# Kernel tuning notes

Measured on AMD Instinct MI355X. Metric: run time of the kernel, lower is better.

## Reference

```python
import jax, jax.numpy as jnp
import numpy as np

B, L, D_MODEL, VQ_DIM, K_CODES = 4, 2048, 1024, 64, 8192
EMA_K, EMA_GAMMA = 5, 0.995


def _huber(a, b):
    # HuberLoss(reduction='none'), delta=1.0
    d = a - b
    ad = jnp.abs(d)
    return jnp.where(ad < 1.0, 0.5 * d * d, ad - 0.5)


def setup_inputs() -> dict:
    key = jax.random.key(0)
    ks = jax.random.split(key, 6)
    h = jax.random.normal(ks[0], (B, L, D_MODEL), dtype=jnp.float32)
    attn_mask = jnp.ones((B, L), dtype=jnp.float32)
    proj_w = jax.random.normal(ks[1], (D_MODEL, VQ_DIM), dtype=jnp.float32) / np.sqrt(D_MODEL)
    proj_b = jnp.zeros((VQ_DIM,), dtype=jnp.float32)
    proj_inv_w = jax.random.normal(ks[2], (VQ_DIM, D_MODEL), dtype=jnp.float32) / np.sqrt(VQ_DIM)
    proj_inv_b = jnp.zeros((D_MODEL,), dtype=jnp.float32)
    emb_weight = jax.random.uniform(ks[3], (K_CODES, VQ_DIM), dtype=jnp.float32,
                                    minval=-1.0 / K_CODES, maxval=1.0 / K_CODES)
    count = jnp.zeros((K_CODES,), dtype=jnp.float32)
    return {"h": h, "attn_mask": attn_mask, "proj_w": proj_w, "proj_b": proj_b,
            "proj_inv_w": proj_inv_w, "proj_inv_b": proj_inv_b,
            "emb_weight": emb_weight, "count": count}


def reference(h, attn_mask, proj_w, proj_b, proj_inv_w, proj_inv_b, emb_weight, count):
    # project + L2-normalize tokens
    hp = h @ proj_w + proj_b                                   # [B, L, vq]
    hp = hp / jnp.linalg.norm(hp, axis=-1, keepdims=True)
    h_flat = hp.reshape(-1, VQ_DIM)                            # [N, vq]
    # L2-normalize codebook (in-place .data normalization in torch)
    E = emb_weight / jnp.linalg.norm(emb_weight, axis=-1, keepdims=True)  # [K, vq]
    # squared-distance via norm expansion
    distances = (jnp.sum(h_flat ** 2, axis=1, keepdims=True)
                 + jnp.sum(E ** 2, axis=1)
                 - 2.0 * h_flat @ E.T)                         # [N, K]
    m = attn_mask.reshape(-1, 1)
    distances = distances * m + 1e7 * (1.0 - m)
    code = jnp.argmin(distances, axis=1).reshape(B, L)         # [B, L]
    quantized = E[code]                                        # gather [B, L, vq]
    # straight-through estimator
    q_ste = hp + jax.lax.stop_gradient(quantized - hp)
    # usage count buffer update (unique+bincount == scatter-add of ones)
    new_count = count.at[code.reshape(-1)].add(1.0)
    # EMA codebook update (train mode): top-k nearest tokens per code
    neg_top, topk_ids = jax.lax.top_k((-distances).T, EMA_K)   # [K, k]
    h_feat = h_flat[topk_ids].mean(axis=1)                     # [K, vq]
    update_mask = jnp.abs(neg_top).min(axis=1) > 0.1           # [K]
    updated = E * EMA_GAMMA + h_feat * (1.0 - EMA_GAMMA)
    new_emb = jnp.where(update_mask[:, None], updated, E)
    # commitment / codebook loss (Huber both ways), masked mean
    loss = _huber(jax.lax.stop_gradient(hp), q_ste) + 0.25 * _huber(hp, jax.lax.stop_gradient(q_ste))
    mw = attn_mask[:, :, None]
    vq_loss = ((loss * mw).sum(axis=1) / mw.sum(axis=1)).mean()
    q_out = q_ste @ proj_inv_w + proj_inv_b                    # [B, L, d_model]
    return q_out, code, vq_loss, new_emb, new_count
```

## Files before the change

kernel.cpp:

```cpp
#include <hip/hip_runtime.h>
#include <float.h>


typedef __attribute__((ext_vector_type(8)))  short bf16x8;
typedef __attribute__((ext_vector_type(16))) float f32x16;

__device__ __forceinline__ unsigned short f2bf(float x) {
  unsigned u = __float_as_uint(x);
  unsigned r = (u + 0x7fffu + ((u >> 16) & 1u)) >> 16;
  return (unsigned short)r;
}
__device__ __forceinline__ float bf2f(unsigned short b) {
  return __uint_as_float(((unsigned)b) << 16);
}
__device__ __forceinline__ size_t frag_off(int e, int ks, int lh) {
  return ((size_t)((((e >> 5) * 4 + ks) * 2 + lh) * 32 + (e & 31))) * 8;
}

__device__ __forceinline__ void kins5(unsigned& s0, unsigned& s1, unsigned& s2,
                                      unsigned& s3, unsigned& s4, unsigned k) {
  unsigned t = k, m;
  m = min(s0, t); t = max(s0, t); s0 = m;
  m = min(s1, t); t = max(s1, t); s1 = m;
  m = min(s2, t); t = max(s2, t); s2 = m;
  m = min(s3, t); t = max(s3, t); s3 = m;
  s4 = min(s4, t);
}
__device__ __forceinline__ void lins5(float& d0, float& d1, float& d2,
                                      float& d3, float& d4, int& i0, int& i1,
                                      int& i2, int& i3, int& i4, float dv,
                                      int iv) {
  if (dv < d4 || (dv == d4 && iv < i4)) {
    d4 = dv; i4 = iv;
    if (d4 < d3 || (d4 == d3 && i4 < i3)) { float t = d3; d3 = d4; d4 = t; int u = i3; i3 = i4; i4 = u; }
    if (d3 < d2 || (d3 == d2 && i3 < i2)) { float t = d2; d2 = d3; d3 = t; int u = i2; i2 = i3; i3 = u; }
    if (d2 < d1 || (d2 == d1 && i2 < i1)) { float t = d1; d1 = d2; d2 = t; int u = i1; i1 = i2; i2 = u; }
    if (d1 < d0 || (d1 == d0 && i1 < i0)) { float t = d0; d0 = d1; d1 = t; int u = i0; i0 = i1; i1 = u; }
  }
}

__global__ __launch_bounds__(256) void k_proj(
    const float* __restrict__ h, const float* __restrict__ w,
    const float* __restrict__ bias, float* __restrict__ hp_norm,
    float* __restrict__ h2, unsigned short* __restrict__ hpH,
    unsigned short* __restrict__ hpL) {
  __shared__ __align__(16) float hs[16 * 68];
  __shared__ __align__(16) float ws[64 * 64];
  const int tid = threadIdx.x;
  const int tb = blockIdx.x * 16;
  const int tok = tid >> 4;
  const int dimg = tid & 15;
  const float4* h4 = (const float4*)h;
  const float4* w4 = (const float4*)w;
  float4* ws4 = (float4*)ws;
  float4 acc = {0.f, 0.f, 0.f, 0.f};
  for (int ch = 0; ch < 16; ++ch) {
    __syncthreads();
    *(float4*)&hs[tok * 68 + dimg * 4] = h4[(size_t)(tb + tok) * 256 + ch * 16 + dimg];
#pragma unroll
    for (int i = 0; i < 4; ++i) {
      int idx = tid + i * 256;
      int k = idx >> 4, dq = idx & 15;
      ws4[k * 16 + dq] = w4[(size_t)(ch * 64 + k) * 16 + dq];
    }
    __syncthreads();
#pragma unroll 8
    for (int k = 0; k < 64; ++k) {
      float hv = hs[tok * 68 + k];
      float4 wv = *(const float4*)&ws[k * 64 + dimg * 4];
      acc.x = fmaf(hv, wv.x, acc.x);
      acc.y = fmaf(hv, wv.y, acc.y);
      acc.z = fmaf(hv, wv.z, acc.z);
      acc.w = fmaf(hv, wv.w, acc.w);
    }
  }
  const float4 bv = ((const float4*)bias)[dimg];
  acc.x += bv.x; acc.y += bv.y; acc.z += bv.z; acc.w += bv.w;
  float sq = acc.x * acc.x + acc.y * acc.y + acc.z * acc.z + acc.w * acc.w;
#pragma unroll
  for (int o = 1; o <= 8; o <<= 1) sq += __shfl_xor(sq, o, 64);
  float nrm = sqrtf(sq);
  float4 vn;
  vn.x = acc.x / nrm; vn.y = acc.y / nrm; vn.z = acc.z / nrm; vn.w = acc.w / nrm;
  ((float4*)hp_norm)[(size_t)(tb + tok) * 16 + dimg] = vn;
  unsigned short hx = f2bf(vn.x), hy = f2bf(vn.y), hz = f2bf(vn.z), hw = f2bf(vn.w);
  uint2 hi_pack, lo_pack;
  hi_pack.x = (unsigned)hx | ((unsigned)hy << 16);
  hi_pack.y = (unsigned)hz | ((unsigned)hw << 16);
  lo_pack.x = (unsigned)f2bf(vn.x - bf2f(hx)) | ((unsigned)f2bf(vn.y - bf2f(hy)) << 16);
  lo_pack.y = (unsigned)f2bf(vn.z - bf2f(hz)) | ((unsigned)f2bf(vn.w - bf2f(hw)) << 16);
  {
    int ks = dimg >> 2, lh = (dimg >> 1) & 1, half = dimg & 1;
    size_t off = frag_off(tb + tok, ks, lh) + half * 4;
    *(uint2*)(hpH + off) = hi_pack;
    *(uint2*)(hpL + off) = lo_pack;
  }
  float s2 = vn.x * vn.x + vn.y * vn.y + vn.z * vn.z + vn.w * vn.w;
#pragma unroll
  for (int o = 1; o <= 8; o <<= 1) s2 += __shfl_xor(s2, o, 64);
  if (dimg == 0) h2[tb + tok] = s2;
}

__global__ __launch_bounds__(256) void k_enorm(
    const float* __restrict__ emb, float* __restrict__ E,
    float* __restrict__ e2, unsigned short* __restrict__ EH,
    unsigned short* __restrict__ EL,
    const float* __restrict__ cnt, float* __restrict__ ncnt,
    const float* __restrict__ wiv, unsigned short* __restrict__ wTH,
    unsigned short* __restrict__ wTL) {
  __shared__ float tile[64][65];
  const int b = blockIdx.x;
  const int tid = threadIdx.x;
  if (b >= 2080) {
    const int n0 = (b - 2080) * 64;
    const float4* w4 = (const float4*)wiv;
#pragma unroll
    for (int i = 0; i < 4; ++i) {
      int idx = tid + i * 256;
      int k = idx >> 4, nq = idx & 15;
      float4 v = w4[k * 256 + (n0 >> 2) + nq];
      tile[nq * 4 + 0][k] = v.x;
      tile[nq * 4 + 1][k] = v.y;
      tile[nq * 4 + 2][k] = v.z;
      tile[nq * 4 + 3][k] = v.w;
    }
    __syncthreads();
    const int n = tid >> 2;
    const int k0 = (tid & 3) * 16;
#pragma unroll
    for (int j = 0; j < 16; j += 4) {
      int k = k0 + j;
      float x0 = tile[n][k], x1 = tile[n][k + 1], x2 = tile[n][k + 2],
            x3 = tile[n][k + 3];
      unsigned short h0 = f2bf(x0), h1 = f2bf(x1), h2_ = f2bf(x2), h3 = f2bf(x3);
      uint2 hp_, lp_;
      hp_.x = (unsigned)h0 | ((unsigned)h1 << 16);
      hp_.y = (unsigned)h2_ | ((unsigned)h3 << 16);
      lp_.x = (unsigned)f2bf(x0 - bf2f(h0)) | ((unsigned)f2bf(x1 - bf2f(h1)) << 16);
      lp_.y = (unsigned)f2bf(x2 - bf2f(h2_)) | ((unsigned)f2bf(x3 - bf2f(h3)) << 16);
      size_t off = frag_off(n0 + n, k >> 4, (k >> 3) & 1) + (k & 7);
      *(uint2*)(wTH + off) = hp_;
      *(uint2*)(wTL + off) = lp_;
    }
    return;
  }
  if (b >= 2048) {
    int i = (b - 2048) * 256 + tid;
    ncnt[i] = cnt[i];
    return;
  }
  const int c = b * 4 + (tid >> 6);
  const int lane = tid & 63;
  float v = emb[(size_t)c * 64 + lane];
  float sq = v * v;
#pragma unroll
  for (int o = 32; o > 0; o >>= 1) sq += __shfl_xor(sq, o, 64);
  float vn = v / sqrtf(sq);
  E[(size_t)c * 64 + lane] = vn;
  unsigned short hb = f2bf(vn);
  size_t off = frag_off(c, lane >> 4, (lane >> 3) & 1) + (lane & 7);
  EH[off] = hb;
  EL[off] = f2bf(vn - bf2f(hb));
  float s2 = vn * vn;
#pragma unroll
  for (int o = 32; o > 0; o >>= 1) s2 += __shfl_xor(s2, o, 64);
  if (lane == 0) e2[c] = s2;
}

__global__ __launch_bounds__(512, 4) void k_argmin(
    const unsigned short* __restrict__ hpH, const unsigned short* __restrict__ hpL,
    const unsigned short* __restrict__ EHg, const unsigned short* __restrict__ ELg,
    const float* __restrict__ e2g,
    float* __restrict__ amin_d, int* __restrict__ amin_c) {
  __shared__ __align__(16) unsigned char buf[2][16384];
  __shared__ float e2l[1024];
  __shared__ float mD[2][128];
  __shared__ int   mC[2][128];
  const int tid = threadIdx.x;
  const int w = tid >> 6, lane = tid & 63;
  const int l31 = lane & 31, lh = lane >> 5;
  const int rowg = w >> 1, colg = w & 1;
  const int tok_base = blockIdx.x * 128;
  const int cstrip = blockIdx.y * 1024;
  const int row_t = tok_base + rowg * 32 + l31;
  bf16x8 aH[4], aL[4];
#pragma unroll
  for (int ks = 0; ks < 4; ++ks) {
    aH[ks] = *(const bf16x8*)(hpH + frag_off(row_t, ks, lh));
    aL[ks] = *(const bf16x8*)(hpL + frag_off(row_t, ks, lh));
  }
  e2l[tid] = e2g[cstrip + tid];
  e2l[tid + 512] = e2g[cstrip + tid + 512];
  float bu[16]; int bc[16];
#pragma unroll
  for (int r = 0; r < 16; ++r) { bu[r] = FLT_MAX; bc[r] = 0x7fffffff; }
  bf16x8 rH, rL;
  {
    size_t gb = (size_t)(blockIdx.y * 32) * 2048 + (size_t)tid * 8;
    rH = *(const bf16x8*)(EHg + gb);
    rL = *(const bf16x8*)(ELg + gb);
    *(bf16x8*)(buf[0] + tid * 16) = rH;
    *(bf16x8*)(buf[0] + 8192 + tid * 16) = rL;
  }
  __syncthreads();
  for (int ch = 0; ch < 16; ++ch) {
    if (ch < 15) {
      size_t gb = (size_t)(blockIdx.y * 32 + (ch + 1) * 2) * 2048 + (size_t)tid * 8;
      rH = *(const bf16x8*)(EHg + gb);
      rL = *(const bf16x8*)(ELg + gb);
    }
    const unsigned char* bcur = buf[ch & 1];
    f32x16 acc = {};
#pragma unroll
    for (int ks = 0; ks < 4; ++ks) {
      const int boff = ((colg * 8 + ks * 2 + lh) * 32 + l31) * 16;
      bf16x8 bL = *(const bf16x8*)(bcur + 8192 + boff);
      bf16x8 bH = *(const bf16x8*)(bcur + boff);
      acc = __builtin_amdgcn_mfma_f32_32x32x16_bf16(aL[ks], bL, acc, 0, 0, 0);
      acc = __builtin_amdgcn_mfma_f32_32x32x16_bf16(aL[ks], bH, acc, 0, 0, 0);
      acc = __builtin_amdgcn_mfma_f32_32x32x16_bf16(aH[ks], bL, acc, 0, 0, 0);
      acc = __builtin_amdgcn_mfma_f32_32x32x16_bf16(aH[ks], bH, acc, 0, 0, 0);
    }
    const int mycode = cstrip + ch * 64 + colg * 32 + l31;
    const float e2c = e2l[ch * 64 + colg * 32 + l31];
#pragma unroll
    for (int r = 0; r < 16; ++r) {
      float u = fmaf(-2.f, acc[r], e2c);
      if (u < bu[r]) { bu[r] = u; bc[r] = mycode; }
    }
    if (ch < 15) {
      *(bf16x8*)(buf[(ch + 1) & 1] + tid * 16) = rH;
      *(bf16x8*)(buf[(ch + 1) & 1] + 8192 + tid * 16) = rL;
    }
    __syncthreads();
  }
#pragma unroll
  for (int r = 0; r < 16; ++r) {
#pragma unroll
    for (int o = 1; o <= 16; o <<= 1) {
      float ou = __shfl_xor(bu[r], o, 64);
      int oc = __shfl_xor(bc[r], o, 64);
      if (ou < bu[r] || (ou == bu[r] && oc < bc[r])) { bu[r] = ou; bc[r] = oc; }
    }
  }
  if (l31 == 0) {
#pragma unroll
    for (int r = 0; r < 16; ++r) {
      const int roff = rowg * 32 + (r & 3) + 8 * (r >> 2) + 4 * lh;
      mD[colg][roff] = bu[r];
      mC[colg][roff] = bc[r];
    }
  }
  __syncthreads();
  if (tid < 128) {
    float d0 = mD[0][tid], d1 = mD[1][tid];
    int c0 = mC[0][tid], c1 = mC[1][tid];
    if (d1 < d0 || (d1 == d0 && c1 < c0)) { d0 = d1; c0 = c1; }
    const int t = tok_base + tid;
    amin_d[(size_t)t * 8 + blockIdx.y] = d0;
    amin_c[(size_t)t * 8 + blockIdx.y] = c0;
  }
}

__global__ __launch_bounds__(512, 4) void k_top5(
    const unsigned short* __restrict__ hpH, const unsigned short* __restrict__ hpL,
    const unsigned short* __restrict__ EHg, const unsigned short* __restrict__ ELg,
    const float* __restrict__ h2g, const float* __restrict__ e2g,
    const float* __restrict__ maskg,
    float* __restrict__ t5d, int* __restrict__ t5i) {
  __shared__ __align__(16) unsigned char buf[2][16384];
  __shared__ __align__(16) float Pl[1024];
  __shared__ float sD[4][2][32][5];
  __shared__ int   sI[4][2][32][5];
  const int tid = threadIdx.x;
  const int w = tid >> 6, lane = tid & 63;
  const int l31 = lane & 31, lh = lane >> 5;
  const int rowg = w >> 2, colg = w & 3;
  const int code_t = blockIdx.x * 128 + colg * 32 + l31;
  const int tstrip = blockIdx.y * 1024;
  bf16x8 bH[4], bL[4];
#pragma unroll
  for (int ks = 0; ks < 4; ++ks) {
    bH[ks] = *(const bf16x8*)(EHg + frag_off(code_t, ks, lh));
    bL[ks] = *(const bf16x8*)(ELg + frag_off(code_t, ks, lh));
  }
  {
    int t0 = tid, t1 = tid + 512;
    float m0 = maskg[tstrip + t0], m1 = maskg[tstrip + t1];
    Pl[t0] = fmaf(h2g[tstrip + t0], m0, 1.0e7f * (1.f - m0) + 4.0f);
    Pl[t1] = fmaf(h2g[tstrip + t1], m1, 1.0e7f * (1.f - m1) + 4.0f);
  }
  unsigned s0 = 0xFFFFFFFFu, s1 = 0xFFFFFFFFu, s2 = 0xFFFFFFFFu,
           s3 = 0xFFFFFFFFu, s4 = 0xFFFFFFFFu;
  bf16x8 rH, rL;
  {
    size_t gb = (size_t)(blockIdx.y * 32) * 2048 + (size_t)tid * 8;
    rH = *(const bf16x8*)(hpH + gb);
    rL = *(const bf16x8*)(hpL + gb);
    *(bf16x8*)(buf[0] + tid * 16) = rH;
    *(bf16x8*)(buf[0] + 8192 + tid * 16) = rL;
  }
  __syncthreads();
  for (int ch = 0; ch < 16; ++ch) {
    if (ch < 15) {
      size_t gb = (size_t)(blockIdx.y * 32 + (ch + 1) * 2) * 2048 + (size_t)tid * 8;
      rH = *(const bf16x8*)(hpH + gb);
      rL = *(const bf16x8*)(hpL + gb);
    }
    const unsigned char* bcur = buf[ch & 1];
    f32x16 acc = {};
#pragma unroll
    for (int ks = 0; ks < 4; ++ks) {
      const int aoff = ((rowg * 8 + ks * 2 + lh) * 32 + l31) * 16;
      bf16x8 aL = *(const bf16x8*)(bcur + 8192 + aoff);
      bf16x8 aH = *(const bf16x8*)(bcur + aoff);
      acc = __builtin_amdgcn_mfma_f32_32x32x16_bf16(aL, bL[ks], acc, 0, 0, 0);
      acc = __builtin_amdgcn_mfma_f32_32x32x16_bf16(aL, bH[ks], acc, 0, 0, 0);
      acc = __builtin_amdgcn_mfma_f32_32x32x16_bf16(aH, bL[ks], acc, 0, 0, 0);
      acc = __builtin_amdgcn_mfma_f32_32x32x16_bf16(aH, bH[ks], acc, 0, 0, 0);
    }
    const int rowb = ch * 64 + rowg * 32 + 4 * lh;
    const unsigned encb = (unsigned)(ch << 4);
#pragma unroll
    for (int rq = 0; rq < 4; ++rq) {
      float4 pl = *(const float4*)&Pl[rowb + 8 * rq];
      float kx = fmaf(-2.f, acc[4 * rq + 0], pl.x);
      kins5(s0, s1, s2, s3, s4,
            (__float_as_uint(kx) & 0xFFFFFF00u) | (encb + 4 * rq + 0));
      float ky = fmaf(-2.f, acc[4 * rq + 1], pl.y);
      kins5(s0, s1, s2, s3, s4,
            (__float_as_uint(ky) & 0xFFFFFF00u) | (encb + 4 * rq + 1));
      float kz = fmaf(-2.f, acc[4 * rq + 2], pl.z);
      kins5(s0, s1, s2, s3, s4,
            (__float_as_uint(kz) & 0xFFFFFF00u) | (encb + 4 * rq + 2));
      float kw = fmaf(-2.f, acc[4 * rq + 3], pl.w);
      kins5(s0, s1, s2, s3, s4,
            (__float_as_uint(kw) & 0xFFFFFF00u) | (encb + 4 * rq + 3));
    }
    if (ch < 15) {
      *(bf16x8*)(buf[(ch + 1) & 1] + tid * 16) = rH;
      *(bf16x8*)(buf[(ch + 1) & 1] + 8192 + tid * 16) = rL;
    }
    __syncthreads();
  }
  float td0, td1, td2, td3, td4;
  int ti0, ti1, ti2, ti3, ti4;
  {
    auto dec = [&](unsigned k, float& d, int& i) {
      d = __uint_as_float(k & 0xFFFFFF00u);
      int enc = (int)(k & 255u);
      int r = enc & 15, chh = enc >> 4;
      i = tstrip + chh * 64 + rowg * 32 + lh * 4 + (r & 3) + 8 * (r >> 2);
    };
    dec(s0, td0, ti0); dec(s1, td1, ti1); dec(s2, td2, ti2);
    dec(s3, td3, ti3); dec(s4, td4, ti4);
  }
  {
    float od0 = __shfl_xor(td0, 32, 64), od1 = __shfl_xor(td1, 32, 64),
          od2 = __shfl_xor(td2, 32, 64), od3 = __shfl_xor(td3, 32, 64),
          od4 = __shfl_xor(td4, 32, 64);
    int oi0 = __shfl_xor(ti0, 32, 64), oi1 = __shfl_xor(ti1, 32, 64),
        oi2 = __shfl_xor(ti2, 32, 64), oi3 = __shfl_xor(ti3, 32, 64),
        oi4 = __shfl_xor(ti4, 32, 64);
    lins5(td0, td1, td2, td3, td4, ti0, ti1, ti2, ti3, ti4, od0, oi0);
    lins5(td0, td1, td2, td3, td4, ti0, ti1, ti2, ti3, ti4, od1, oi1);
    lins5(td0, td1, td2, td3, td4, ti0, ti1, ti2, ti3, ti4, od2, oi2);
    lins5(td0, td1, td2, td3, td4, ti0, ti1, ti2, ti3, ti4, od3, oi3);
    lins5(td0, td1, td2, td3, td4, ti0, ti1, ti2, ti3, ti4, od4, oi4);
  }
  if (lane < 32) {
    sD[colg][rowg][l31][0] = td0; sD[colg][rowg][l31][1] = td1;
    sD[colg][rowg][l31][2] = td2; sD[colg][rowg][l31][3] = td3;
    sD[colg][rowg][l31][4] = td4;
    sI[colg][rowg][l31][0] = ti0; sI[colg][rowg][l31][1] = ti1;
    sI[colg][rowg][l31][2] = ti2; sI[colg][rowg][l31][3] = ti3;
    sI[colg][rowg][l31][4] = ti4;
  }
  __syncthreads();
  if (tid < 128) {
    const int cg = tid >> 5, cl = tid & 31;
    float rd0 = sD[cg][0][cl][0], rd1 = sD[cg][0][cl][1],
          rd2 = sD[cg][0][cl][2], rd3 = sD[cg][0][cl][3],
          rd4 = sD[cg][0][cl][4];
    int ri0 = sI[cg][0][cl][0], ri1 = sI[cg][0][cl][1],
        ri2 = sI[cg][0][cl][2], ri3 = sI[cg][0][cl][3],
        ri4 = sI[cg][0][cl][4];
#pragma unroll
    for (int s = 0; s < 5; ++s)
      lins5(rd0, rd1, rd2, rd3, rd4, ri0, ri1, ri2, ri3, ri4,
            sD[cg][1][cl][s], sI[cg][1][cl][s]);
    const int code = blockIdx.x * 128 + tid;
    const float sh = e2g[code] - 4.0f;
    size_t gb = (size_t)code * 40 + (size_t)blockIdx.y * 5;
    t5d[gb + 0] = rd0 + sh; t5i[gb + 0] = ri0;
    t5d[gb + 1] = rd1 + sh; t5i[gb + 1] = ri1;
    t5d[gb + 2] = rd2 + sh; t5i[gb + 2] = ri2;
    t5d[gb + 3] = rd3 + sh; t5i[gb + 3] = ri3;
    t5d[gb + 4] = rd4 + sh; t5i[gb + 4] = ri4;
  }
}

__global__ __launch_bounds__(256) void k_code(
    const float* __restrict__ amin_d, const int* __restrict__ amin_c,
    const float* __restrict__ hp, const float* __restrict__ E,
    const float* __restrict__ maskg,
    float* __restrict__ code_f, int* __restrict__ code_i,
    float* __restrict__ newcount, float* __restrict__ loss_tok) {
  const int wid = threadIdx.x >> 6;
  const int lane = threadIdx.x & 63;
  const int t = blockIdx.x * 4 + wid;
  float d = FLT_MAX;
  int c = 0x7fffffff;
  if (lane < 8) {
    d = amin_d[(size_t)t * 8 + lane];
    c = amin_c[(size_t)t * 8 + lane];
  }
#pragma unroll
  for (int o = 1; o <= 4; o <<= 1) {
    float od = __shfl_xor(d, o, 64);
    int oc = __shfl_xor(c, o, 64);
    if (od < d || (od == d && oc < c)) { d = od; c = oc; }
  }
  c = __shfl(c, 0, 64);
  if (maskg[t] == 0.f) c = 0;
  float a = hp[(size_t)t * 64 + lane];
  float e = E[(size_t)c * 64 + lane];
  float q = a + (e - a);
  float df = a - q;
  float ad = fabsf(df);
  float l = ad < 1.f ? 0.5f * df * df : ad - 0.5f;
#pragma unroll
  for (int o = 32; o > 0; o >>= 1) l += __shfl_xor(l, o, 64);
  if (lane == 0) {
    code_f[t] = (float)c;
    code_i[t] = c;
    loss_tok[t] = l;
    atomicAdd(&newcount[c], 1.0f);
  }
}

__global__ __launch_bounds__(256, 2) void k_qout(
    const int* __restrict__ code_i,
    const unsigned short* __restrict__ EH, const unsigned short* __restrict__ EL,
    const unsigned short* __restrict__ wTH, const unsigned short* __restrict__ wTL,
    const float* __restrict__ bias, float* __restrict__ qout) {
  const int tid = threadIdx.x;
  const int w = tid >> 6, lane = tid & 63;
  const int l31 = lane & 31, lh = lane >> 5;
  const int rowg = w >> 1, colg = w & 1;
  const int tok_base = blockIdx.x * 64;
  const int col_base = blockIdx.y * 64;
  const int row_t = tok_base + rowg * 32 + l31;
  const int c = code_i[row_t];
  const int n = col_base + colg * 32 + l31;
  bf16x8 aH[4], aL[4], bH[4], bL[4];
#pragma unroll
  for (int ks = 0; ks < 4; ++ks) {
    aH[ks] = *(const bf16x8*)(EH + frag_off(c, ks, lh));
    aL[ks] = *(const bf16x8*)(EL + frag_off(c, ks, lh));
    bH[ks] = *(const bf16x8*)(wTH + frag_off(n, ks, lh));
    bL[ks] = *(const bf16x8*)(wTL + frag_off(n, ks, lh));
  }
  f32x16 c0 = {}, c1 = {}, c2 = {}, c3 = {};
#pragma unroll
  for (int ks = 0; ks < 4; ++ks) {
    c0 = __builtin_amdgcn_mfma_f32_32x32x16_bf16(aL[ks], bL[ks], c0, 0, 0, 0);
    c1 = __builtin_amdgcn_mfma_f32_32x32x16_bf16(aL[ks], bH[ks], c1, 0, 0, 0);
    c2 = __builtin_amdgcn_mfma_f32_32x32x16_bf16(aH[ks], bL[ks], c2, 0, 0, 0);
    c3 = __builtin_amdgcn_mfma_f32_32x32x16_bf16(aH[ks], bH[ks], c3, 0, 0, 0);
  }
  const float bc = bias[n];
#pragma unroll
  for (int r = 0; r < 16; ++r) {
    int row = rowg * 32 + (r & 3) + 8 * (r >> 2) + 4 * lh;
    float dot = ((c0[r] + c1[r]) + c2[r]) + c3[r];
    qout[(size_t)(tok_base + row) * 1024 + n] = dot + bc;
  }
}

__global__ __launch_bounds__(256) void k_emb(
    const float* __restrict__ t5d, const int* __restrict__ t5i,
    const float* __restrict__ hp, const float* __restrict__ E,
    float* __restrict__ newemb,
    const float* __restrict__ loss_tok, const float* __restrict__ maskg,
    float* __restrict__ vq) {
  __shared__ float S[256], M[256];
  const int tid = threadIdx.x;
  if (blockIdx.x == 2048) {
    float s = 0.f, m = 0.f;
    const int base = tid * 32;
    for (int i = 0; i < 32; ++i) {
      float mm = maskg[base + i];
      s = fmaf(loss_tok[base + i], mm, s);
      m += mm;
    }
    S[tid] = s; M[tid] = m;
    __syncthreads();
    if (tid == 0) {
      float tot = 0.f;
      for (int b = 0; b < 4; ++b) {
        float sb = 0.f, mb = 0.f;
        for (int i = 0; i < 64; ++i) { sb += S[b * 64 + i]; mb += M[b * 64 + i]; }
        tot += sb / mb;
      }
      vq[0] = tot * 1.25f / 256.0f;
    }
    return;
  }
  const int wid = tid >> 6;
  const int lane = tid & 63;
  const int c = blockIdx.x * 4 + wid;
  float d = FLT_MAX;
  int idx = 0x7fffffff;
  if (lane < 40) {
    d = t5d[(size_t)c * 40 + lane];
    idx = t5i[(size_t)c * 40 + lane];
  }
  float seld[5]; int sel[5];
#pragma unroll
  for (int r = 0; r < 5; ++r) {
    float bd = d; int bi = idx;
#pragma unroll
    for (int o = 1; o <= 32; o <<= 1) {
      float od = __shfl_xor(bd, o, 64);
      int oi = __shfl_xor(bi, o, 64);
      if (od < bd || (od == bd && oi < bi)) { bd = od; bi = oi; }
    }
    seld[r] = bd; sel[r] = bi;
    if (idx == bi) d = FLT_MAX;
  }
  float m5 = fabsf(seld[0]);
#pragma unroll
  for (int r = 1; r < 5; ++r) m5 = fminf(m5, fabsf(seld[r]));
  float hf = 0.f;
#pragma unroll
  for (int r = 0; r < 5; ++r) hf += hp[(size_t)sel[r] * 64 + lane];
  hf = hf / 5.0f;
  float ev = E[(size_t)c * 64 + lane];
  float outv = (m5 > 0.1f) ? (ev * 0.995f + hf * (float)(1.0 - 0.995)) : ev;
  newemb[(size_t)c * 64 + lane] = outv;
}

extern "C" void kernel_launch(void* const* d_in, const int* in_sizes, int n_in,
                              void* d_out, int out_size, void* d_ws,
                              size_t ws_size, hipStream_t stream) {
  (void)in_sizes; (void)n_in; (void)out_size; (void)ws_size;
  const float* h          = (const float*)d_in[0];
  const float* mask       = (const float*)d_in[1];
  const float* proj_w     = (const float*)d_in[2];
  const float* proj_b     = (const float*)d_in[3];
  const float* proj_inv_w = (const float*)d_in[4];
  const float* proj_inv_b = (const float*)d_in[5];
  const float* emb        = (const float*)d_in[6];
  const float* count      = (const float*)d_in[7];

  float* out      = (float*)d_out;
  float* q_out    = out;
  float* code_f   = out + 8388608;
  float* vq       = out + 8396800;
  float* newemb   = out + 8396801;
  float* newcount = out + 8921089;

  float* ws = (float*)d_ws;
  float* hp_norm        = ws;
  float* h2             = ws + 524288;
  float* E              = ws + 532480;
  float* e2             = ws + 1056768;
  unsigned short* hpH   = (unsigned short*)(ws + 1064960);
  unsigned short* hpL   = (unsigned short*)(ws + 1327104);
  unsigned short* EH    = (unsigned short*)(ws + 1589248);
  unsigned short* EL    = (unsigned short*)(ws + 1851392);
  unsigned short* wTH   = (unsigned short*)(ws + 2113536);
  unsigned short* wTL   = (unsigned short*)(ws + 2146304);
  float* amin_d         = ws + 2179072;
  int*   amin_c         = (int*)(ws + 2244608);
  int*   code_i         = (int*)(ws + 2310144);
  float* t5d            = ws + 2318336;
  int*   t5i            = (int*)(ws + 2646016);
  float* loss_tok       = ws + 2973696;

  k_proj<<<512, 256, 0, stream>>>(h, proj_w, proj_b, hp_norm, h2, hpH, hpL);
  k_enorm<<<2096, 256, 0, stream>>>(emb, E, e2, EH, EL, count, newcount,
                                    proj_inv_w, wTH, wTL);
  k_argmin<<<dim3(64, 8), 512, 0, stream>>>(hpH, hpL, EH, EL, e2,
                                            amin_d, amin_c);
  k_top5<<<dim3(64, 8), 512, 0, stream>>>(hpH, hpL, EH, EL, h2, e2, mask,
                                          t5d, t5i);
  k_code<<<2048, 256, 0, stream>>>(amin_d, amin_c, hp_norm, E, mask,
                                   code_f, code_i, newcount, loss_tok);
  k_qout<<<dim3(128, 16), 256, 0, stream>>>(code_i, EH, EL, wTH, wTL,
                                            proj_inv_b, q_out);
  k_emb<<<2049, 256, 0, stream>>>(t5d, t5i, hp_norm, E, newemb,
                                  loss_tok, mask, vq);
}
```

Baseline: 155.4 us.

## Split distance kernels into 16 strips and stage tiles via direct global-to-LDS loads

The argmin and top-5 kernels now split the reduction dimension into 16 strips instead of 8, doubling the grid to 1024 blocks with half the chunks per block. Tile staging uses global_load_lds so data goes straight into shared memory without passing through registers, and the reduction scratch arrays now reuse the staging buffer to cut shared-memory use. The downstream merge kernels are changed to combine 16 partial results per token and 80 candidates per code. The aim is more parallelism, more resident blocks per CU and lower register pressure. The cost is more partial results to write and merge, and reliance on the async LDS load finishing before the barrier.

```diff
diff --git a/kernel.cpp b/kernel.cpp
--- a/kernel.cpp
+++ b/kernel.cpp
@@ -4,6 +4,11 @@
 
 typedef __attribute__((ext_vector_type(8)))  short bf16x8;
 typedef __attribute__((ext_vector_type(16))) float f32x16;
+
+#define GLDS16(gp, lp)                                              \
+  __builtin_amdgcn_global_load_lds(                                 \
+      (const __attribute__((address_space(1))) void*)(gp),          \
+      (__attribute__((address_space(3))) void*)(lp), 16, 0, 0)
 
 __device__ __forceinline__ unsigned short f2bf(float x) {
   unsigned u = __float_as_uint(x);
@@ -172,16 +177,18 @@
     const unsigned short* __restrict__ EHg, const unsigned short* __restrict__ ELg,
     const float* __restrict__ e2g,
     float* __restrict__ amin_d, int* __restrict__ amin_c) {
-  __shared__ __align__(16) unsigned char buf[2][16384];
-  __shared__ float e2l[1024];
-  __shared__ float mD[2][128];
-  __shared__ int   mC[2][128];
+  __shared__ __align__(16) unsigned char smem[2 * 16384 + 2048];
+  unsigned char* buf0 = smem;
+  unsigned char* buf1 = smem + 16384;
+  float* e2l = (float*)(smem + 32768);
+  float* mD = (float*)smem;
+  int*   mC = (int*)(smem + 1024);
   const int tid = threadIdx.x;
   const int w = tid >> 6, lane = tid & 63;
   const int l31 = lane & 31, lh = lane >> 5;
   const int rowg = w >> 1, colg = w & 1;
   const int tok_base = blockIdx.x * 128;
-  const int cstrip = blockIdx.y * 1024;
+  const int cstrip = blockIdx.y * 512;
   const int row_t = tok_base + rowg * 32 + l31;
   bf16x8 aH[4], aL[4];
 #pragma unroll
@@ -190,26 +197,23 @@
     aL[ks] = *(const bf16x8*)(hpL + frag_off(row_t, ks, lh));
   }
   e2l[tid] = e2g[cstrip + tid];
-  e2l[tid + 512] = e2g[cstrip + tid + 512];
   float bu[16]; int bc[16];
 #pragma unroll
   for (int r = 0; r < 16; ++r) { bu[r] = FLT_MAX; bc[r] = 0x7fffffff; }
-  bf16x8 rH, rL;
   {
-    size_t gb = (size_t)(blockIdx.y * 32) * 2048 + (size_t)tid * 8;
-    rH = *(const bf16x8*)(EHg + gb);
-    rL = *(const bf16x8*)(ELg + gb);
-    *(bf16x8*)(buf[0] + tid * 16) = rH;
-    *(bf16x8*)(buf[0] + 8192 + tid * 16) = rL;
+    size_t gb = (size_t)(blockIdx.y * 16) * 2048 + (size_t)tid * 8;
+    GLDS16(EHg + gb, buf0 + tid * 16);
+    GLDS16(ELg + gb, buf0 + 8192 + tid * 16);
   }
   __syncthreads();
-  for (int ch = 0; ch < 16; ++ch) {
-    if (ch < 15) {
-      size_t gb = (size_t)(blockIdx.y * 32 + (ch + 1) * 2) * 2048 + (size_t)tid * 8;
-      rH = *(const bf16x8*)(EHg + gb);
-      rL = *(const bf16x8*)(ELg + gb);
-    }
-    const unsigned char* bcur = buf[ch & 1];
+  for (int ch = 0; ch < 8; ++ch) {
+    const unsigned char* bcur = (ch & 1) ? buf1 : buf0;
+    unsigned char* bnxt = (ch & 1) ? buf0 : buf1;
+    if (ch < 7) {
+      size_t gb = (size_t)(blockIdx.y * 16 + (ch + 1) * 2) * 2048 + (size_t)tid * 8;
+      GLDS16(EHg + gb, bnxt + tid * 16);
+      GLDS16(ELg + gb, bnxt + 8192 + tid * 16);
+    }
     f32x16 acc = {};
 #pragma unroll
     for (int ks = 0; ks < 4; ++ks) {
@@ -228,10 +232,6 @@
       float u = fmaf(-2.f, acc[r], e2c);
       if (u < bu[r]) { bu[r] = u; bc[r] = mycode; }
     }
-    if (ch < 15) {
-      *(bf16x8*)(buf[(ch + 1) & 1] + tid * 16) = rH;
-      *(bf16x8*)(buf[(ch + 1) & 1] + 8192 + tid * 16) = rL;
-    }
     __syncthreads();
   }
 #pragma unroll
@@ -247,18 +247,18 @@
 #pragma unroll
     for (int r = 0; r < 16; ++r) {
       const int roff = rowg * 32 + (r & 3) + 8 * (r >> 2) + 4 * lh;
-      mD[colg][roff] = bu[r];
-      mC[colg][roff] = bc[r];
+      mD[colg * 128 + roff] = bu[r];
+      mC[colg * 128 + roff] = bc[r];
     }
   }
   __syncthreads();
   if (tid < 128) {
-    float d0 = mD[0][tid], d1 = mD[1][tid];
-    int c0 = mC[0][tid], c1 = mC[1][tid];
+    float d0 = mD[tid], d1 = mD[128 + tid];
+    int c0 = mC[tid], c1 = mC[128 + tid];
     if (d1 < d0 || (d1 == d0 && c1 < c0)) { d0 = d1; c0 = c1; }
     const int t = tok_base + tid;
-    amin_d[(size_t)t * 8 + blockIdx.y] = d0;
-    amin_c[(size_t)t * 8 + blockIdx.y] = c0;
+    amin_d[(size_t)t * 16 + blockIdx.y] = d0;
+    amin_c[(size_t)t * 16 + blockIdx.y] = c0;
   }
 }
 
@@ -268,16 +268,18 @@
     const float* __restrict__ h2g, const float* __restrict__ e2g,
     const float* __restrict__ maskg,
     float* __restrict__ t5d, int* __restrict__ t5i) {
-  __shared__ __align__(16) unsigned char buf[2][16384];
-  __shared__ __align__(16) float Pl[1024];
-  __shared__ float sD[4][2][32][5];
-  __shared__ int   sI[4][2][32][5];
+  __shared__ __align__(16) unsigned char smem[2 * 16384 + 2048];
+  unsigned char* buf0 = smem;
+  unsigned char* buf1 = smem + 16384;
+  float* Pl = (float*)(smem + 32768);
+  float* sD = (float*)smem;
+  int*   sI = (int*)(smem + 5120);
   const int tid = threadIdx.x;
   const int w = tid >> 6, lane = tid & 63;
   const int l31 = lane & 31, lh = lane >> 5;
   const int rowg = w >> 2, colg = w & 3;
   const int code_t = blockIdx.x * 128 + colg * 32 + l31;
-  const int tstrip = blockIdx.y * 1024;
+  const int tstrip = blockIdx.y * 512;
   bf16x8 bH[4], bL[4];
 #pragma unroll
   for (int ks = 0; ks < 4; ++ks) {
@@ -285,29 +287,25 @@
     bL[ks] = *(const bf16x8*)(ELg + frag_off(code_t, ks, lh));
   }
   {
-    int t0 = tid, t1 = tid + 512;
-    float m0 = maskg[tstrip + t0], m1 = maskg[tstrip + t1];
-    Pl[t0] = fmaf(h2g[tstrip + t0], m0, 1.0e7f * (1.f - m0) + 4.0f);
-    Pl[t1] = fmaf(h2g[tstrip + t1], m1, 1.0e7f * (1.f - m1) + 4.0f);
+    float m0 = maskg[tstrip + tid];
+    Pl[tid] = fmaf(h2g[tstrip + tid], m0, 1.0e7f * (1.f - m0) + 4.0f);
   }
   unsigned s0 = 0xFFFFFFFFu, s1 = 0xFFFFFFFFu, s2 = 0xFFFFFFFFu,
            s3 = 0xFFFFFFFFu, s4 = 0xFFFFFFFFu;
-  bf16x8 rH, rL;
   {
-    size_t gb = (size_t)(blockIdx.y * 32) * 2048 + (size_t)tid * 8;
-    rH = *(const bf16x8*)(hpH + gb);
-    rL = *(const bf16x8*)(hpL + gb);
-    *(bf16x8*)(buf[0] + tid * 16) = rH;
-    *(bf16x8*)(buf[0] + 8192 + tid * 16) = rL;
+    size_t gb = (size_t)(blockIdx.y * 16) * 2048 + (size_t)tid * 8;
+    GLDS16(hpH + gb, buf0 + tid * 16);
+    GLDS16(hpL + gb, buf0 + 8192 + tid * 16);
   }
   __syncthreads();
-  for (int ch = 0; ch < 16; ++ch) {
-    if (ch < 15) {
-      size_t gb = (size_t)(blockIdx.y * 32 + (ch + 1) * 2) * 2048 + (size_t)tid * 8;
-      rH = *(const bf16x8*)(hpH + gb);
-      rL = *(const bf16x8*)(hpL + gb);
-    }
-    const unsigned char* bcur = buf[ch & 1];
+  for (int ch = 0; ch < 8; ++ch) {
+    const unsigned char* bcur = (ch & 1) ? buf1 : buf0;
+    unsigned char* bnxt = (ch & 1) ? buf0 : buf1;
+    if (ch < 7) {
+      size_t gb = (size_t)(blockIdx.y * 16 + (ch + 1) * 2) * 2048 + (size_t)tid * 8;
+      GLDS16(hpH + gb, bnxt + tid * 16);
+      GLDS16(hpL + gb, bnxt + 8192 + tid * 16);
+    }
     f32x16 acc = {};
 #pragma unroll
     for (int ks = 0; ks < 4; ++ks) {
@@ -337,10 +335,6 @@
       kins5(s0, s1, s2, s3, s4,
             (__float_as_uint(kw) & 0xFFFFFF00u) | (encb + 4 * rq + 3));
     }
-    if (ch < 15) {
-      *(bf16x8*)(buf[(ch + 1) & 1] + tid * 16) = rH;
-      *(bf16x8*)(buf[(ch + 1) & 1] + 8192 + tid * 16) = rL;
-    }
     __syncthreads();
   }
   float td0, td1, td2, td3, td4;
@@ -369,29 +363,26 @@
     lins5(td0, td1, td2, td3, td4, ti0, ti1, ti2, ti3, ti4, od4, oi4);
   }
   if (lane < 32) {
-    sD[colg][rowg][l31][0] = td0; sD[colg][rowg][l31][1] = td1;
-    sD[colg][rowg][l31][2] = td2; sD[colg][rowg][l31][3] = td3;
-    sD[colg][rowg][l31][4] = td4;
-    sI[colg][rowg][l31][0] = ti0; sI[colg][rowg][l31][1] = ti1;
-    sI[colg][rowg][l31][2] = ti2; sI[colg][rowg][l31][3] = ti3;
-    sI[colg][rowg][l31][4] = ti4;
+    float* sd = sD + (((colg * 2 + rowg) * 32) + l31) * 5;
+    int* si = sI + (((colg * 2 + rowg) * 32) + l31) * 5;
+    sd[0] = td0; sd[1] = td1; sd[2] = td2; sd[3] = td3; sd[4] = td4;
+    si[0] = ti0; si[1] = ti1; si[2] = ti2; si[3] = ti3; si[4] = ti4;
   }
   __syncthreads();
   if (tid < 128) {
     const int cg = tid >> 5, cl = tid & 31;
-    float rd0 = sD[cg][0][cl][0], rd1 = sD[cg][0][cl][1],
-          rd2 = sD[cg][0][cl][2], rd3 = sD[cg][0][cl][3],
-          rd4 = sD[cg][0][cl][4];
-    int ri0 = sI[cg][0][cl][0], ri1 = sI[cg][0][cl][1],
-        ri2 = sI[cg][0][cl][2], ri3 = sI[cg][0][cl][3],
-        ri4 = sI[cg][0][cl][4];
+    const float* s0p = sD + ((cg * 2 + 0) * 32 + cl) * 5;
+    const int* s0i = sI + ((cg * 2 + 0) * 32 + cl) * 5;
+    const float* s1p = sD + ((cg * 2 + 1) * 32 + cl) * 5;
+    const int* s1i = sI + ((cg * 2 + 1) * 32 + cl) * 5;
+    float rd0 = s0p[0], rd1 = s0p[1], rd2 = s0p[2], rd3 = s0p[3], rd4 = s0p[4];
+    int ri0 = s0i[0], ri1 = s0i[1], ri2 = s0i[2], ri3 = s0i[3], ri4 = s0i[4];
 #pragma unroll
     for (int s = 0; s < 5; ++s)
-      lins5(rd0, rd1, rd2, rd3, rd4, ri0, ri1, ri2, ri3, ri4,
-            sD[cg][1][cl][s], sI[cg][1][cl][s]);
+      lins5(rd0, rd1, rd2, rd3, rd4, ri0, ri1, ri2, ri3, ri4, s1p[s], s1i[s]);
     const int code = blockIdx.x * 128 + tid;
     const float sh = e2g[code] - 4.0f;
-    size_t gb = (size_t)code * 40 + (size_t)blockIdx.y * 5;
+    size_t gb = (size_t)code * 80 + (size_t)blockIdx.y * 5;
     t5d[gb + 0] = rd0 + sh; t5i[gb + 0] = ri0;
     t5d[gb + 1] = rd1 + sh; t5i[gb + 1] = ri1;
     t5d[gb + 2] = rd2 + sh; t5i[gb + 2] = ri2;
@@ -411,12 +402,12 @@
   const int t = blockIdx.x * 4 + wid;
   float d = FLT_MAX;
   int c = 0x7fffffff;
-  if (lane < 8) {
-    d = amin_d[(size_t)t * 8 + lane];
-    c = amin_c[(size_t)t * 8 + lane];
-  }
-#pragma unroll
-  for (int o = 1; o <= 4; o <<= 1) {
+  if (lane < 16) {
+    d = amin_d[(size_t)t * 16 + lane];
+    c = amin_c[(size_t)t * 16 + lane];
+  }
+#pragma unroll
+  for (int o = 1; o <= 8; o <<= 1) {
     float od = __shfl_xor(d, o, 64);
     int oc = __shfl_xor(c, o, 64);
     if (od < d || (od == d && oc < c)) { d = od; c = oc; }
@@ -510,16 +501,18 @@
   const int wid = tid >> 6;
   const int lane = tid & 63;
   const int c = blockIdx.x * 4 + wid;
-  float d = FLT_MAX;
-  int idx = 0x7fffffff;
-  if (lane < 40) {
-    d = t5d[(size_t)c * 40 + lane];
-    idx = t5i[(size_t)c * 40 + lane];
-  }
+  size_t base = (size_t)c * 80;
+  float dA = t5d[base + lane];
+  int iA = t5i[base + lane];
+  float dB = FLT_MAX;
+  int iB = 0x7fffffff;
+  if (lane < 16) { dB = t5d[base + 64 + lane]; iB = t5i[base + 64 + lane]; }
   float seld[5]; int sel[5];
 #pragma unroll
   for (int r = 0; r < 5; ++r) {
-    float bd = d; int bi = idx;
+    bool bsel = (dB < dA) || (dB == dA && iB < iA);
+    float bd = bsel ? dB : dA;
+    int bi = bsel ? iB : iA;
 #pragma unroll
     for (int o = 1; o <= 32; o <<= 1) {
       float od = __shfl_xor(bd, o, 64);
@@ -527,7 +520,8 @@
       if (od < bd || (od == bd && oi < bi)) { bd = od; bi = oi; }
     }
     seld[r] = bd; sel[r] = bi;
-    if (idx == bi) d = FLT_MAX;
+    if (iA == bi) dA = FLT_MAX;
+    if (iB == bi) dB = FLT_MAX;
   }
   float m5 = fabsf(seld[0]);
 #pragma unroll
@@ -573,19 +567,19 @@
   unsigned short* wTH   = (unsigned short*)(ws + 2113536);
   unsigned short* wTL   = (unsigned short*)(ws + 2146304);
   float* amin_d         = ws + 2179072;
-  int*   amin_c         = (int*)(ws + 2244608);
-  int*   code_i         = (int*)(ws + 2310144);
-  float* t5d            = ws + 2318336;
-  int*   t5i            = (int*)(ws + 2646016);
-  float* loss_tok       = ws + 2973696;
+  int*   amin_c         = (int*)(ws + 2310144);
+  int*   code_i         = (int*)(ws + 2441216);
+  float* t5d            = ws + 2449408;
+  int*   t5i            = (int*)(ws + 3104768);
+  float* loss_tok       = ws + 3760128;
 
   k_proj<<<512, 256, 0, stream>>>(h, proj_w, proj_b, hp_norm, h2, hpH, hpL);
   k_enorm<<<2096, 256, 0, stream>>>(emb, E, e2, EH, EL, count, newcount,
                                     proj_inv_w, wTH, wTL);
-  k_argmin<<<dim3(64, 8), 512, 0, stream>>>(hpH, hpL, EH, EL, e2,
-                                            amin_d, amin_c);
-  k_top5<<<dim3(64, 8), 512, 0, stream>>>(hpH, hpL, EH, EL, h2, e2, mask,
-                                          t5d, t5i);
+  k_argmin<<<dim3(64, 16), 512, 0, stream>>>(hpH, hpL, EH, EL, e2,
+                                             amin_d, amin_c);
+  k_top5<<<dim3(64, 16), 512, 0, stream>>>(hpH, hpL, EH, EL, h2, e2, mask,
+                                           t5d, t5i);
   k_code<<<2048, 256, 0, stream>>>(amin_d, amin_c, hp_norm, E, mask,
                                    code_f, code_i, newcount, loss_tok);
   k_qout<<<dim3(128, 16), 256, 0, stream>>>(code_i, EH, EL, wTH, wTL,
```

Result: slower. 166.7 us (median of 3 runs) (+7.2%).
